# Kernel optimization log

Hardware: AMD Instinct MI355X
Metric: run time of the kernel (lower is better)

Reference implementation:

```python
import jax, jax.numpy as jnp
import numpy as np

EMB_DIM = 128
MID = 192  # ceil(1.5 * emb_dim)
VOCAB = 3000
KCLS = 5
B = 16
S = 128
EPS = 1e-5


def _linear_init(k, fin, fout):
    k1, k2 = jax.random.split(k)
    bound = 1.0 / np.sqrt(fin)
    W = jax.random.uniform(k1, (fin, fout), minval=-bound, maxval=bound, dtype=jnp.float32)
    b = jax.random.uniform(k2, (fout,), minval=-bound, maxval=bound, dtype=jnp.float32)
    return W, b


def setup_inputs() -> dict:
    key = jax.random.key(0)
    ks = jax.random.split(key, 7)
    emb = jax.random.normal(ks[0], (VOCAB, EMB_DIM), dtype=jnp.float32)
    W1, b1 = _linear_init(ks[1], 2 * EMB_DIM, MID)   # encoder layer 1
    W2, b2 = _linear_init(ks[2], MID, EMB_DIM)       # encoder layer 2
    W3, b3 = _linear_init(ks[3], EMB_DIM, MID)       # decoder layer 1
    W4, b4 = _linear_init(ks[4], MID, 2 * EMB_DIM)   # decoder layer 2
    Wk, bk = _linear_init(ks[5], EMB_DIM, KCLS)      # soft head
    inputs = jax.random.randint(ks[6], (B, S), 0, VOCAB, dtype=jnp.int64)
    return dict(inputs=inputs, emb=emb, W1=W1, b1=b1, W2=W2, b2=b2,
                W3=W3, b3=b3, W4=W4, b4=b4, Wk=Wk, bk=bk)


def _forward(inputs, emb, W1, b1, W2, b2, W3, b3, W4, b4, Wk, bk):
    X = emb[inputs]                      # (B,S,m)
    Bs, Sl, m = X.shape
    bidx = jnp.arange(Bs)
    karr = jnp.arange(Sl)
    jarr = jnp.arange(Sl - 1)

    def step(carry, t):
        nodes, counts, acc = carry       # (B,S,m), (B,S), (B,)
        L = Sl - t                       # current active list length
        right, left = nodes[:, 1:], nodes[:, :-1]          # pair j = (node[j+1], node[j])
        y = (jnp.concatenate([right, left], -1) @ W1 + b1) @ W2 + b2   # (B,S-1,m)
        xx = (y @ W3 + b3) @ W4 + b4                                    # (B,S-1,2m)
        # torch cross_entropy with float-vector target: -sum(target * log_softmax(input))
        ls1 = -(right * jax.nn.log_softmax(xx[..., :m], -1)).sum(-1)
        ls2 = -(left * jax.nn.log_softmax(xx[..., m:], -1)).sum(-1)
        n1, n2 = counts[:, 1:], counts[:, :-1]
        loss = ((n1 + EPS) * ls1 + (n2 + EPS) * ls2) / (n1 + n2 + EPS)
        valid = jarr < (L - 1)                                          # only first L-1 pairs active
        idx = jnp.argmin(jnp.where(valid[None, :], loss, jnp.inf), axis=1)  # (B,)
        acc = acc + jnp.take_along_axis(loss, idx[:, None], 1)[:, 0]
        father_x = jnp.take_along_axis(y, idx[:, None, None], 1)[:, 0]  # (B,m)
        # faithful bug: lc = nodelist[idx-1] (python wrap to L-1 when idx==0), rc = nodelist[idx]
        lc_idx = jnp.where(idx == 0, L - 1, idx - 1)
        father_cnt = (jnp.take_along_axis(counts, idx[:, None], 1)[:, 0]
                      + jnp.take_along_axis(counts, lc_idx[:, None], 1)[:, 0])
        pos = jnp.maximum(idx - 1, 0)
        # new list: drop lc and rc, father lands at pos; gather map reproduces list insert/remove
        src = jnp.where((idx[:, None] == 0) | (karr[None, :] < idx[:, None] - 1),
                        karr[None, :], karr[None, :] + 1)
        src = jnp.minimum(src, Sl - 1)
        nodes = jnp.take_along_axis(nodes, src[:, :, None], 1).at[bidx, pos].set(father_x)
        counts = jnp.take_along_axis(counts, src, 1).at[bidx, pos].set(father_cnt)
        return (nodes, counts, acc), None

    init = (X, jnp.ones((Bs, Sl), X.dtype), jnp.zeros((Bs,), X.dtype))
    (nodes, counts, acc), _ = jax.lax.scan(step, init, jnp.arange(Sl - 1))
    pred = jnp.argmax(nodes[:, 0] @ Wk + bk, axis=-1)   # argmax softmax == argmax logits
    return pred, acc.sum() / Bs


def reference(inputs, emb, W1, b1, W2, b2, W3, b3, W4, b4, Wk, bk):
    return _forward(inputs, emb, W1, b1, W2, b2, W3, b3, W4, b4, Wk, bk)
```

## Files before the change

kernel.cpp:

```cpp
#include <hip/hip_runtime.h>
#include <math.h>

#define EMB 128
#define MID 192
#define SEQ 128
#define BATCH 16
#define NPAIR 127
#define KCLS 5
#define EPSF 1e-5f

#define OFF_WYT   0
#define OFF_BY    32768
#define OFF_WXXT  32896
#define OFF_BXX   65664
#define OFF_NODES 65920
#define OFF_YC    328064
#define OFF_L0    588160

__global__ void k_comp(const float* __restrict__ W1, const float* __restrict__ b1,
                       const float* __restrict__ W2, const float* __restrict__ b2,
                       const float* __restrict__ W3, const float* __restrict__ b3,
                       const float* __restrict__ W4, const float* __restrict__ b4,
                       float* __restrict__ ws) {
    int tid = blockIdx.x * blockDim.x + threadIdx.x;
    if (tid < 32768) {
        int k = tid >> 7, o = tid & 127;
        float a = 0.f;
        for (int j = 0; j < MID; ++j) a += W1[k*MID+j] * W2[j*EMB+o];
        int q = k >> 6, jj = k & 63;
        ws[OFF_WYT + (size_t)(o*4 + q)*64 + jj] = a;
    } else if (tid < 65536) {
        int t = tid - 32768;
        int k = t >> 8, c = t & 255;
        float a = 0.f;
        for (int j = 0; j < MID; ++j) a += W3[k*MID+j] * W4[j*256+c];
        int hh = k >> 6, jj = k & 63;
        ws[OFF_WXXT + (size_t)(c*2 + hh)*64 + jj] = a;
    } else if (tid < 65536 + 128) {
        int o = tid - 65536;
        float a = b2[o];
        for (int j = 0; j < MID; ++j) a += b1[j] * W2[j*EMB+o];
        ws[OFF_BY + o] = a;
    } else if (tid < 65536 + 128 + 256) {
        int o = tid - 65536 - 128;
        float a = b4[o];
        for (int j = 0; j < MID; ++j) a += b3[j] * W4[j*256+o];
        ws[OFF_BXX + o] = a;
    }
}

__global__ void k_nodes(const int* __restrict__ inp, const float* __restrict__ emb,
                        float* __restrict__ ws) {
    int tid = blockIdx.x * blockDim.x + threadIdx.x;
    if (tid >= BATCH*SEQ*EMB) return;
    int d = tid & 127;
    int bs = tid >> 7;
    int tok = inp[bs];
    ws[OFF_NODES + tid] = emb[tok*EMB + d];
}

#define PIN64(arr) { _Pragma("unroll") for (int _i = 0; _i < 64; ++_i) asm volatile("" : "+v"(arr[_i])); }

__global__ void __launch_bounds__(512, 1) k_init(float* __restrict__ ws) {
    __shared__ float s_x[2][2*EMB];
    __shared__ float s_red[4][2][EMB];
    __shared__ float s_redx[2][2][256];
    __shared__ float s_y[2][EMB];
    __shared__ float s_by[EMB];
    __shared__ float s_bxx[2*EMB];
    __shared__ float s_ls[2][2];
    int tid = threadIdx.x;
    int b = blockIdx.x >> 3, g = blockIdx.x & 7;
    float wy[64], wxx[64];
    {
        const float4* gw = (const float4*)(ws + OFF_WYT) + ((size_t)(tid & 127)*4 + (tid >> 7))*16;
        #pragma unroll
        for (int i = 0; i < 16; ++i) { float4 v = gw[i]; wy[4*i]=v.x; wy[4*i+1]=v.y; wy[4*i+2]=v.z; wy[4*i+3]=v.w; }
        const float4* gx = (const float4*)(ws + OFF_WXXT) + ((size_t)(tid & 255)*2 + (tid >> 8))*16;
        #pragma unroll
        for (int i = 0; i < 16; ++i) { float4 v = gx[i]; wxx[4*i]=v.x; wxx[4*i+1]=v.y; wxx[4*i+2]=v.z; wxx[4*i+3]=v.w; }
    }
    PIN64(wy); PIN64(wxx);
    if (tid < EMB) s_by[tid] = ws[OFF_BY + tid];
    if (tid < 2*EMB) s_bxx[tid] = ws[OFF_BXX + tid];
    const float* nodes = ws + OFF_NODES + (size_t)b*SEQ*EMB;
    float* yc = ws + OFF_YC + (size_t)b*NPAIR*EMB;
    int q4 = tid >> 7, o = tid & 127;
    int hh = tid >> 8, c = tid & 255;
    int p_s = tid >> 8, kk = tid & 255;
    __syncthreads();
    for (int i = 0; i < 8; ++i) {
        int base = g*16 + i*2;
        {
            int j = base + p_s;
            int jj = j < NPAIR ? j : NPAIR - 1;
            s_x[p_s][kk] = nodes[(jj + (kk < 128 ? 1 : 0))*EMB + (kk & 127)];
        }
        __syncthreads();
        float a0 = 0.f, a1 = 0.f;
        #pragma unroll
        for (int j = 0; j < 64; ++j) {
            float w = wy[j];
            a0 += s_x[0][q4*64 + j] * w;
            a1 += s_x[1][q4*64 + j] * w;
        }
        s_red[q4][0][o] = a0;
        s_red[q4][1][o] = a1;
        __syncthreads();
        if (tid < 256) {
            int p = tid >> 7, oo = tid & 127;
            float yv = s_red[0][p][oo] + s_red[1][p][oo] + s_red[2][p][oo] + s_red[3][p][oo] + s_by[oo];
            s_y[p][oo] = yv;
            int j2 = base + p;
            if (j2 < NPAIR) yc[(size_t)j2*EMB + oo] = yv;
        }
        __syncthreads();
        float c0 = 0.f, c1 = 0.f;
        #pragma unroll
        for (int j = 0; j < 64; ++j) {
            float w = wxx[j];
            c0 += s_y[0][hh*64 + j] * w;
            c1 += s_y[1][hh*64 + j] * w;
        }
        s_redx[hh][0][c] = c0;
        s_redx[hh][1][c] = c1;
        __syncthreads();
        if (tid < 256) {
            int w = tid >> 6, lane = tid & 63;
            int p2 = w >> 1, h2 = w & 1;
            int cA = h2*128 + lane, cB = cA + 64;
            float v0 = s_redx[0][p2][cA] + s_redx[1][p2][cA] + s_bxx[cA];
            float v1 = s_redx[0][p2][cB] + s_redx[1][p2][cB] + s_bxx[cB];
            float m = fmaxf(v0, v1);
            for (int s = 32; s; s >>= 1) m = fmaxf(m, __shfl_xor(m, s, 64));
            float se = expf(v0 - m) + expf(v1 - m);
            for (int s = 32; s; s >>= 1) se += __shfl_xor(se, s, 64);
            float lse = m + logf(se);
            float o0 = s_x[p2][cA], o1 = s_x[p2][cB];
            float term = o0*(v0 - lse) + o1*(v1 - lse);
            for (int s = 32; s; s >>= 1) term += __shfl_xor(term, s, 64);
            if (lane == 0) s_ls[p2][h2] = -term;
        }
        __syncthreads();
        if (tid < 2) {
            int j2 = base + tid;
            if (j2 < NPAIR) {
                float l = ((1.f+EPSF)*s_ls[tid][0] + (1.f+EPSF)*s_ls[tid][1]) / (2.f + EPSF);
                ws[OFF_L0 + b*NPAIR + j2] = l;
            }
        }
        __syncthreads();
    }
}

#define SX(p, c) s_x[p][(((c) >> 6)*72) + ((c) & 63)]

__global__ void __launch_bounds__(512, 1) k_seq(float* __restrict__ ws,
                      const float* __restrict__ Wk, const float* __restrict__ bkv,
                      float* __restrict__ out) {
    __shared__ float s_nodes[SEQ*EMB];
    __shared__ float s_yc[NPAIR*EMB];
    __shared__ float s_x[2][4*72];
    __shared__ float s_y[2][EMB];
    __shared__ float s_xx[2][2*EMB];
    __shared__ float s_by[EMB];
    __shared__ float s_bxx[2*EMB];
    __shared__ float s_ls[2][2];
    __shared__ float s_loss[2][SEQ];
    __shared__ float s_cnt[2][SEQ];
    __shared__ int   s_nslot[2][SEQ];
    __shared__ int   s_yslot[2][SEQ];
    __shared__ float s_restv[2];
    __shared__ int   s_resti[2];
    __shared__ float s_log[KCLS];

    int tid = threadIdx.x;
    int b = blockIdx.x;
    float wy[64], wxx[64];
    {
        const float4* gw = (const float4*)(ws + OFF_WYT) + (size_t)tid*16;
        #pragma unroll
        for (int i = 0; i < 16; ++i) { float4 v = gw[i]; wy[4*i]=v.x; wy[4*i+1]=v.y; wy[4*i+2]=v.z; wy[4*i+3]=v.w; }
        const float4* gx = (const float4*)(ws + OFF_WXXT) + (size_t)tid*16;
        #pragma unroll
        for (int i = 0; i < 16; ++i) { float4 v = gx[i]; wxx[4*i]=v.x; wxx[4*i+1]=v.y; wxx[4*i+2]=v.z; wxx[4*i+3]=v.w; }
    }
    PIN64(wy); PIN64(wxx);
    {
        const float4* gn = (const float4*)(ws + OFF_NODES + (size_t)b*SEQ*EMB);
        float4* sn = (float4*)s_nodes;
        for (int i = tid; i < SEQ*EMB/4; i += 512) sn[i] = gn[i];
        const float4* gy = (const float4*)(ws + OFF_YC + (size_t)b*NPAIR*EMB);
        float4* sy = (float4*)s_yc;
        for (int i = tid; i < NPAIR*EMB/4; i += 512) sy[i] = gy[i];
    }
    if (tid < EMB) s_by[tid] = ws[OFF_BY + tid];
    if (tid < 2*EMB) s_bxx[tid] = ws[OFF_BXX + tid];
    if (tid < NPAIR) { s_loss[0][tid] = ws[OFF_L0 + b*NPAIR + tid]; s_yslot[0][tid] = tid; }
    if (tid < SEQ)   { s_cnt[0][tid] = 1.f; s_nslot[0][tid] = tid; }

    float acc = 0.f;
    int cur = 0;
    int q0c = -1, q1c = -1;
    int slotFr = 0, ysIr = 0, myslot = 0;
    bool stageYc = false;
    const int q4 = tid & 3,  oy = tid >> 2;
    const int hh = tid & 1,  cx = tid >> 1;
    const int sp = tid >> 8, skk = tid & 255;
    __syncthreads();

    #pragma unroll 1
    for (int t = 0; t < NPAIR; ++t) {
        const int L = SEQ - t;
        if (t > 0) {
            if (tid < EMB) s_nodes[slotFr*EMB + tid] = s_yc[(size_t)ysIr*EMB + tid];
            {
                float xv = stageYc ? s_yc[(size_t)ysIr*EMB + (skk & 127)]
                                   : s_nodes[myslot*EMB + (skk & 127)];
                s_x[sp][((skk >> 6)*72) + (skk & 63)] = xv;
            }
            __syncthreads();
            {
                float a0 = 0.f, a1 = 0.f;
                const float* x0 = &s_x[0][q4*72];
                const float* x1 = &s_x[1][q4*72];
                #pragma unroll
                for (int j = 0; j < 64; ++j) { float w = wy[j]; a0 += x0[j]*w; a1 += x1[j]*w; }
                a0 += __shfl_xor(a0, 1, 64); a1 += __shfl_xor(a1, 1, 64);
                a0 += __shfl_xor(a0, 2, 64); a1 += __shfl_xor(a1, 2, 64);
                if (q4 == 0) {
                    float bb = s_by[oy];
                    float y0 = a0 + bb, y1 = a1 + bb;
                    s_y[0][oy] = y0; s_y[1][oy] = y1;
                    s_yc[(size_t)s_yslot[cur][q0c]*EMB + oy] = y0;
                    s_yc[(size_t)s_yslot[cur][q1c]*EMB + oy] = y1;
                }
            }
            __syncthreads();
            {
                float c0 = 0.f, c1 = 0.f;
                const float* y0p = &s_y[0][hh*64];
                const float* y1p = &s_y[1][hh*64];
                #pragma unroll
                for (int j = 0; j < 64; ++j) { float w = wxx[j]; c0 += y0p[j]*w; c1 += y1p[j]*w; }
                c0 += __shfl_xor(c0, 1, 64); c1 += __shfl_xor(c1, 1, 64);
                if (hh == 0) {
                    float bb = s_bxx[cx];
                    s_xx[0][cx] = c0 + bb;
                    s_xx[1][cx] = c1 + bb;
                }
            }
            __syncthreads();
        }
        if (t > 0 && tid < 128) {
            int p2 = tid >> 6, h2 = (tid >> 5) & 1, l5 = tid & 31;
            int base = h2*128 + l5;
            float v0 = s_xx[p2][base],      v1 = s_xx[p2][base+32];
            float v2 = s_xx[p2][base+64],   v3 = s_xx[p2][base+96];
            float o0 = SX(p2, base),        o1 = SX(p2, base+32);
            float o2 = SX(p2, base+64),     o3 = SX(p2, base+96);
            float m   = fmaxf(fmaxf(v0, v1), fmaxf(v2, v3));
            float sov = v0*o0 + v1*o1 + v2*o2 + v3*o3;
            float so  = (o0 + o1) + (o2 + o3);
            for (int s = 16; s; s >>= 1) {
                m    = fmaxf(m, __shfl_xor(m, s, 64));
                sov += __shfl_xor(sov, s, 64);
                so  += __shfl_xor(so, s, 64);
            }
            float se = expf(v0 - m) + expf(v1 - m) + expf(v2 - m) + expf(v3 - m);
            for (int s = 16; s; s >>= 1) se += __shfl_xor(se, s, 64);
            if (l5 == 0) s_ls[p2][h2] = (m + logf(se))*so - sov;
        } else if (tid >= 128 && tid < 256) {
            int j = tid - 128;
            float v = (j <= L-2 && j != q0c && j != q1c) ? s_loss[cur][j] : INFINITY;
            int ii = j;
            for (int s = 32; s; s >>= 1) {
                float ov = __shfl_xor(v, s, 64);
                int   oi = __shfl_xor(ii, s, 64);
                if (ov < v || (ov == v && oi < ii)) { v = ov; ii = oi; }
            }
            if ((tid & 63) == 0) { s_restv[(tid >> 6) - 2] = v; s_resti[(tid >> 6) - 2] = ii; }
        }
        __syncthreads();
        float l0 = INFINITY, l1 = INFINITY;
        if (t > 0) {
            float n1a = s_cnt[cur][q0c+1], n2a = s_cnt[cur][q0c];
            l0 = ((n1a + EPSF)*s_ls[0][0] + (n2a + EPSF)*s_ls[0][1]) / (n1a + n2a + EPSF);
            float n1b = s_cnt[cur][q1c+1], n2b = s_cnt[cur][q1c];
            l1 = ((n1b + EPSF)*s_ls[1][0] + (n2b + EPSF)*s_ls[1][1]) / (n1b + n2b + EPSF);
        }
        float bv = s_restv[0]; int bi = s_resti[0];
        {
            float rv = s_restv[1]; int ri = s_resti[1];
            if (rv < bv || (rv == bv && ri < bi)) { bv = rv; bi = ri; }
        }
        if (t > 0) {
            if (l1 < bv || (l1 == bv && q1c < bi)) { bv = l1; bi = q1c; }
            if (l0 < bv || (l0 == bv && q0c < bi)) { bv = l0; bi = q0c; }
        }
        if (tid == 0) acc += bv;
        const int idx = bi;
        const int pos = idx > 0 ? idx - 1 : 0;
        const bool dS = idx > 0;
        const float fcnt = s_cnt[cur][idx] + s_cnt[cur][idx == 0 ? L-1 : idx-1];
        slotFr = s_nslot[cur][pos];
        ysIr   = s_yslot[cur][idx];
        const int nxt = cur ^ 1;
        if (tid < NPAIR) {
            int sh = (dS && tid >= pos+1 && tid <= L-3) ? 1 : 0;
            int sj = tid + sh;
            float v = (sj == q0c) ? l0 : (sj == q1c) ? l1 : s_loss[cur][sj];
            s_loss[nxt][tid]  = v;
            s_yslot[nxt][tid] = s_yslot[cur][sj];
        }
        if (tid < SEQ) {
            int sh = (dS && tid >= pos+1 && tid <= L-2) ? 1 : 0;
            s_cnt[nxt][tid]   = (tid == pos) ? fcnt : s_cnt[cur][tid + sh];
            s_nslot[nxt][tid] = s_nslot[cur][tid + sh];
        }
        q0c = pos >= 1 ? pos - 1 : 0;
        q1c = pos;
        {
            int qq = (sp ? q1c : q0c) + (skk < 128 ? 1 : 0);
            stageYc = (qq == q1c);
            int sh = (dS && qq >= pos+1 && qq <= L-2) ? 1 : 0;
            myslot = s_nslot[cur][qq + sh];
        }
        cur = nxt;
        __syncthreads();
    }
    {
        int w = tid >> 6, l = tid & 63;
        if (w < KCLS) {
            const float* root = s_yc + (size_t)ysIr*EMB;
            float p = root[2*l]*Wk[(2*l)*KCLS + w] + root[2*l+1]*Wk[(2*l+1)*KCLS + w];
            for (int s = 32; s; s >>= 1) p += __shfl_xor(p, s, 64);
            if (l == 0) s_log[w] = p + bkv[w];
        }
    }
    __syncthreads();
    if (tid == 0) {
        int best = 0;
        for (int cc = 1; cc < KCLS; ++cc) if (s_log[cc] > s_log[best]) best = cc;
        out[b] = (float)best;
        atomicAdd(&out[BATCH], acc * (1.f/16.f));
    }
}

extern "C" void kernel_launch(void* const* d_in, const int* in_sizes, int n_in,
                              void* d_out, int out_size, void* d_ws, size_t ws_size,
                              hipStream_t stream) {
    const int*   inp = (const int*)d_in[0];
    const float* emb = (const float*)d_in[1];
    const float* W1  = (const float*)d_in[2];
    const float* b1  = (const float*)d_in[3];
    const float* W2  = (const float*)d_in[4];
    const float* b2  = (const float*)d_in[5];
    const float* W3  = (const float*)d_in[6];
    const float* b3  = (const float*)d_in[7];
    const float* W4  = (const float*)d_in[8];
    const float* b4  = (const float*)d_in[9];
    const float* Wk  = (const float*)d_in[10];
    const float* bk  = (const float*)d_in[11];
    float* out = (float*)d_out;
    float* ws  = (float*)d_ws;

    hipMemsetAsync(d_out, 0, (size_t)out_size * sizeof(float), stream);

    k_comp<<<(65920 + 255) / 256, 256, 0, stream>>>(W1, b1, W2, b2, W3, b3, W4, b4, ws);
    k_nodes<<<(BATCH*SEQ*EMB + 255) / 256, 256, 0, stream>>>(inp, emb, ws);
    k_init<<<BATCH * 8, 512, 0, stream>>>(ws);
    k_seq<<<BATCH, 512, 0, stream>>>(ws, Wk, bk, out);
}
```

Before: 543.8 us.

## Split k_seq into two 512-thread groups, each holding one weight matrix, and trim barriers

The block grows from 512 to 1024 threads, with each half keeping only one 64-float weight slice in registers (group 0 the encoder product, group 1 the decoder product), which halves per-thread register pressure. The argmin over the remaining losses now overlaps with the first matvec. Staging the next step's inputs moves into the end-of-step phase, so one barrier per step disappears. In exchange the block has 16 waves instead of 8, so each barrier must gather more waves, and half the threads sit idle during each matvec.

```diff
diff --git a/kernel.cpp b/kernel.cpp
--- a/kernel.cpp
+++ b/kernel.cpp
@@ -155,7 +155,7 @@
 
 #define SX(p, c) s_x[p][(((c) >> 6)*72) + ((c) & 63)]
 
-__global__ void __launch_bounds__(512, 1) k_seq(float* __restrict__ ws,
+__global__ void __launch_bounds__(1024, 1) k_seq(float* __restrict__ ws,
                       const float* __restrict__ Wk, const float* __restrict__ bkv,
                       float* __restrict__ out) {
     __shared__ float s_nodes[SEQ*EMB];
@@ -176,23 +176,21 @@
 
     int tid = threadIdx.x;
     int b = blockIdx.x;
-    float wy[64], wxx[64];
+    const int grp = tid >> 9, lt = tid & 511;
+    float w64[64];
     {
-        const float4* gw = (const float4*)(ws + OFF_WYT) + (size_t)tid*16;
-        #pragma unroll
-        for (int i = 0; i < 16; ++i) { float4 v = gw[i]; wy[4*i]=v.x; wy[4*i+1]=v.y; wy[4*i+2]=v.z; wy[4*i+3]=v.w; }
-        const float4* gx = (const float4*)(ws + OFF_WXXT) + (size_t)tid*16;
-        #pragma unroll
-        for (int i = 0; i < 16; ++i) { float4 v = gx[i]; wxx[4*i]=v.x; wxx[4*i+1]=v.y; wxx[4*i+2]=v.z; wxx[4*i+3]=v.w; }
-    }
-    PIN64(wy); PIN64(wxx);
+        const float4* g = (const float4*)(ws + (grp ? OFF_WXXT : OFF_WYT)) + (size_t)lt*16;
+        #pragma unroll
+        for (int i = 0; i < 16; ++i) { float4 v = g[i]; w64[4*i]=v.x; w64[4*i+1]=v.y; w64[4*i+2]=v.z; w64[4*i+3]=v.w; }
+    }
+    PIN64(w64);
     {
         const float4* gn = (const float4*)(ws + OFF_NODES + (size_t)b*SEQ*EMB);
         float4* sn = (float4*)s_nodes;
-        for (int i = tid; i < SEQ*EMB/4; i += 512) sn[i] = gn[i];
+        for (int i = tid; i < SEQ*EMB/4; i += 1024) sn[i] = gn[i];
         const float4* gy = (const float4*)(ws + OFF_YC + (size_t)b*NPAIR*EMB);
         float4* sy = (float4*)s_yc;
-        for (int i = tid; i < NPAIR*EMB/4; i += 512) sy[i] = gy[i];
+        for (int i = tid; i < NPAIR*EMB/4; i += 1024) sy[i] = gy[i];
     }
     if (tid < EMB) s_by[tid] = ws[OFF_BY + tid];
     if (tid < 2*EMB) s_bxx[tid] = ws[OFF_BXX + tid];
@@ -204,28 +202,21 @@
     int q0c = -1, q1c = -1;
     int slotFr = 0, ysIr = 0, myslot = 0;
     bool stageYc = false;
-    const int q4 = tid & 3,  oy = tid >> 2;
-    const int hh = tid & 1,  cx = tid >> 1;
-    const int sp = tid >> 8, skk = tid & 255;
+    const int q4 = lt & 3,  oy = lt >> 2;
+    const int hh = lt & 1,  cx = lt >> 1;
+    const int sp = lt >> 8, skk = lt & 255;
     __syncthreads();
 
     #pragma unroll 1
     for (int t = 0; t < NPAIR; ++t) {
         const int L = SEQ - t;
         if (t > 0) {
-            if (tid < EMB) s_nodes[slotFr*EMB + tid] = s_yc[(size_t)ysIr*EMB + tid];
-            {
-                float xv = stageYc ? s_yc[(size_t)ysIr*EMB + (skk & 127)]
-                                   : s_nodes[myslot*EMB + (skk & 127)];
-                s_x[sp][((skk >> 6)*72) + (skk & 63)] = xv;
-            }
-            __syncthreads();
-            {
+            if (grp == 0) {
                 float a0 = 0.f, a1 = 0.f;
                 const float* x0 = &s_x[0][q4*72];
                 const float* x1 = &s_x[1][q4*72];
                 #pragma unroll
-                for (int j = 0; j < 64; ++j) { float w = wy[j]; a0 += x0[j]*w; a1 += x1[j]*w; }
+                for (int j = 0; j < 64; ++j) { float w = w64[j]; a0 += x0[j]*w; a1 += x1[j]*w; }
                 a0 += __shfl_xor(a0, 1, 64); a1 += __shfl_xor(a1, 1, 64);
                 a0 += __shfl_xor(a0, 2, 64); a1 += __shfl_xor(a1, 2, 64);
                 if (q4 == 0) {
@@ -235,14 +226,23 @@
                     s_yc[(size_t)s_yslot[cur][q0c]*EMB + oy] = y0;
                     s_yc[(size_t)s_yslot[cur][q1c]*EMB + oy] = y1;
                 }
+            } else if (lt < 128) {
+                float v = (lt <= L-2 && lt != q0c && lt != q1c) ? s_loss[cur][lt] : INFINITY;
+                int ii = lt;
+                for (int s = 32; s; s >>= 1) {
+                    float ov = __shfl_xor(v, s, 64);
+                    int   oi = __shfl_xor(ii, s, 64);
+                    if (ov < v || (ov == v && oi < ii)) { v = ov; ii = oi; }
+                }
+                if ((lt & 63) == 0) { s_restv[lt >> 6] = v; s_resti[lt >> 6] = ii; }
             }
             __syncthreads();
-            {
+            if (grp == 1) {
                 float c0 = 0.f, c1 = 0.f;
                 const float* y0p = &s_y[0][hh*64];
                 const float* y1p = &s_y[1][hh*64];
                 #pragma unroll
-                for (int j = 0; j < 64; ++j) { float w = wxx[j]; c0 += y0p[j]*w; c1 += y1p[j]*w; }
+                for (int j = 0; j < 64; ++j) { float w = w64[j]; c0 += y0p[j]*w; c1 += y1p[j]*w; }
                 c0 += __shfl_xor(c0, 1, 64); c1 += __shfl_xor(c1, 1, 64);
                 if (hh == 0) {
                     float bb = s_bxx[cx];
@@ -251,37 +251,39 @@
                 }
             }
             __syncthreads();
-        }
-        if (t > 0 && tid < 128) {
-            int p2 = tid >> 6, h2 = (tid >> 5) & 1, l5 = tid & 31;
-            int base = h2*128 + l5;
-            float v0 = s_xx[p2][base],      v1 = s_xx[p2][base+32];
-            float v2 = s_xx[p2][base+64],   v3 = s_xx[p2][base+96];
-            float o0 = SX(p2, base),        o1 = SX(p2, base+32);
-            float o2 = SX(p2, base+64),     o3 = SX(p2, base+96);
-            float m   = fmaxf(fmaxf(v0, v1), fmaxf(v2, v3));
-            float sov = v0*o0 + v1*o1 + v2*o2 + v3*o3;
-            float so  = (o0 + o1) + (o2 + o3);
-            for (int s = 16; s; s >>= 1) {
-                m    = fmaxf(m, __shfl_xor(m, s, 64));
-                sov += __shfl_xor(sov, s, 64);
-                so  += __shfl_xor(so, s, 64);
-            }
-            float se = expf(v0 - m) + expf(v1 - m) + expf(v2 - m) + expf(v3 - m);
-            for (int s = 16; s; s >>= 1) se += __shfl_xor(se, s, 64);
-            if (l5 == 0) s_ls[p2][h2] = (m + logf(se))*so - sov;
-        } else if (tid >= 128 && tid < 256) {
-            int j = tid - 128;
-            float v = (j <= L-2 && j != q0c && j != q1c) ? s_loss[cur][j] : INFINITY;
-            int ii = j;
-            for (int s = 32; s; s >>= 1) {
-                float ov = __shfl_xor(v, s, 64);
-                int   oi = __shfl_xor(ii, s, 64);
-                if (ov < v || (ov == v && oi < ii)) { v = ov; ii = oi; }
-            }
-            if ((tid & 63) == 0) { s_restv[(tid >> 6) - 2] = v; s_resti[(tid >> 6) - 2] = ii; }
-        }
-        __syncthreads();
+            if (tid < 128) {
+                int p2 = tid >> 6, h2 = (tid >> 5) & 1, l5 = tid & 31;
+                int base = h2*128 + l5;
+                float v0 = s_xx[p2][base],      v1 = s_xx[p2][base+32];
+                float v2 = s_xx[p2][base+64],   v3 = s_xx[p2][base+96];
+                float o0 = SX(p2, base),        o1 = SX(p2, base+32);
+                float o2 = SX(p2, base+64),     o3 = SX(p2, base+96);
+                float m   = fmaxf(fmaxf(v0, v1), fmaxf(v2, v3));
+                float sov = v0*o0 + v1*o1 + v2*o2 + v3*o3;
+                float so  = (o0 + o1) + (o2 + o3);
+                for (int s = 16; s; s >>= 1) {
+                    m    = fmaxf(m, __shfl_xor(m, s, 64));
+                    sov += __shfl_xor(sov, s, 64);
+                    so  += __shfl_xor(so, s, 64);
+                }
+                float se = expf(v0 - m) + expf(v1 - m) + expf(v2 - m) + expf(v3 - m);
+                for (int s = 16; s; s >>= 1) se += __shfl_xor(se, s, 64);
+                if (l5 == 0) s_ls[p2][h2] = (m + logf(se))*so - sov;
+            }
+            __syncthreads();
+        } else {
+            if (grp == 1 && lt < 128) {
+                float v = (lt <= L-2) ? s_loss[cur][lt] : INFINITY;
+                int ii = lt;
+                for (int s = 32; s; s >>= 1) {
+                    float ov = __shfl_xor(v, s, 64);
+                    int   oi = __shfl_xor(ii, s, 64);
+                    if (ov < v || (ov == v && oi < ii)) { v = ov; ii = oi; }
+                }
+                if ((lt & 63) == 0) { s_restv[lt >> 6] = v; s_resti[lt >> 6] = ii; }
+            }
+            __syncthreads();
+        }
         float l0 = INFINITY, l1 = INFINITY;
         if (t > 0) {
             float n1a = s_cnt[cur][q0c+1], n2a = s_cnt[cur][q0c];
@@ -320,11 +322,16 @@
         }
         q0c = pos >= 1 ? pos - 1 : 0;
         q1c = pos;
-        {
+        if (grp == 0) {
             int qq = (sp ? q1c : q0c) + (skk < 128 ? 1 : 0);
             stageYc = (qq == q1c);
             int sh = (dS && qq >= pos+1 && qq <= L-2) ? 1 : 0;
             myslot = s_nslot[cur][qq + sh];
+            float xv = stageYc ? s_yc[(size_t)ysIr*EMB + (skk & 127)]
+                               : s_nodes[myslot*EMB + (skk & 127)];
+            s_x[sp][((skk >> 6)*72) + (skk & 63)] = xv;
+        } else if (lt < 128) {
+            s_nodes[slotFr*EMB + lt] = s_yc[(size_t)ysIr*EMB + lt];
         }
         cur = nxt;
         __syncthreads();
@@ -370,5 +377,5 @@
     k_comp<<<(65920 + 255) / 256, 256, 0, stream>>>(W1, b1, W2, b2, W3, b3, W4, b4, ws);
     k_nodes<<<(BATCH*SEQ*EMB + 255) / 256, 256, 0, stream>>>(inp, emb, ws);
     k_init<<<BATCH * 8, 512, 0, stream>>>(ws);
-    k_seq<<<BATCH, 512, 0, stream>>>(ws, Wk, bk, out);
-}
+    k_seq<<<BATCH, 1024, 0, stream>>>(ws, Wk, bk, out);
+}
```

New measurement: 573.0 us. 1.05x slower.
